# Performance work log

Hardware: AMD Instinct MI355X
Metric: run time of the kernel (lower is better)

Reference implementation:

```python
import jax, jax.numpy as jnp
import numpy as np
from jax.ops import segment_sum, segment_max

D = 64; H = 2; L = 3
N = 50000; G = 128; E = 600000; NE = 300000
EPS_GEN = 1e-7; EPS_LN = 1e-5


def _lin(key, fan_in, shape):
    return jax.random.normal(key, shape, jnp.float32) / np.sqrt(fan_in)


def setup_inputs() -> dict:
    key = jax.random.key(0)
    ks = iter(jax.random.split(key, 40))
    HD = H * D
    inp = {}
    inp['x'] = jax.random.normal(next(ks), (N, D), jnp.float32)
    inp['cond'] = jax.random.normal(next(ks), (G, D), jnp.float32)
    inp['edge_attr'] = jax.random.normal(next(ks), (E, D), jnp.float32)
    inp['edge_index'] = jax.random.randint(next(ks), (2, E), 0, N)
    inp['non_edge_index'] = jax.random.randint(next(ks), (2, NE), 0, N)
    inp['batch'] = jnp.sort(jax.random.randint(next(ks), (N,), 0, G))
    # per-layer stacked params (L leading dim)
    inp['gen_w'] = _lin(next(ks), D, (L, D, D)); inp['gen_b'] = 0.01 * jax.random.normal(next(ks), (L, D), jnp.float32)
    inp['q_w'] = _lin(next(ks), 2 * D, (L, 2 * D, HD)); inp['q_b'] = 0.01 * jax.random.normal(next(ks), (L, HD), jnp.float32)
    inp['k_w'] = _lin(next(ks), 2 * D, (L, 2 * D, HD)); inp['k_b'] = 0.01 * jax.random.normal(next(ks), (L, HD), jnp.float32)
    inp['v_w'] = _lin(next(ks), 2 * D, (L, 2 * D, HD)); inp['v_b'] = 0.01 * jax.random.normal(next(ks), (L, HD), jnp.float32)
    inp['e_w'] = _lin(next(ks), D, (L, D, HD))  # lin_edge has no bias in TransformerConv
    inp['skip_w'] = _lin(next(ks), 2 * D, (L, 2 * D, HD)); inp['skip_b'] = 0.01 * jax.random.normal(next(ks), (L, HD), jnp.float32)
    inp['lin_w'] = _lin(next(ks), HD, (L, HD, D)); inp['lin_b'] = 0.01 * jax.random.normal(next(ks), (L, D), jnp.float32)
    inp['ff_w1'] = _lin(next(ks), D, (L, D, 4 * D)); inp['ff_b1'] = 0.01 * jax.random.normal(next(ks), (L, 4 * D), jnp.float32)
    inp['ff_w2'] = _lin(next(ks), 4 * D, (L, 4 * D, D)); inp['ff_b2'] = 0.01 * jax.random.normal(next(ks), (L, D), jnp.float32)
    return inp


def graph_layernorm(x, batch, num_graphs):
    # PyG LayerNorm(mode='graph', affine=False): mean/var over all nodes AND features of each graph
    cnt = segment_sum(jnp.ones((x.shape[0],), x.dtype), batch, num_segments=num_graphs)
    norm = jnp.maximum(cnt, 1.0) * x.shape[-1]  # [G]
    mean = segment_sum(x, batch, num_segments=num_graphs).sum(-1) / norm
    xc = x - mean[batch][:, None]
    var = segment_sum(xc * xc, batch, num_segments=num_graphs).sum(-1) / norm
    return xc / jnp.sqrt(var + EPS_LN)[batch][:, None]


def gen_conv(x, src, dst, e, w, b, n):
    # GENConv(d,d,num_layers=1,aggr='add',norm=None): mlp(sum_j relu(x_j + e_ij) + eps  +  x_i)
    msg = jax.nn.relu(x[src] + e) + EPS_GEN
    agg = segment_sum(msg, dst, num_segments=n)
    return (agg + x) @ w + b


def trans_conv(x, src, dst, e, qw, qb, kw, kb, vw, vb, ew, sw, sb, n):
    # TransformerConv(2d, d, heads=H, edge_dim=d, concat=True, root_weight=True)
    q = (x @ qw + qb).reshape(n, H, D)
    k = (x @ kw + kb).reshape(n, H, D)
    v = (x @ vw + vb).reshape(n, H, D)
    ee = (e @ ew).reshape(-1, H, D)
    kj = k[src] + ee
    alpha = jnp.einsum('ehd,ehd->eh', q[dst], kj) / np.sqrt(D)  # [E,H]
    m = segment_max(alpha, dst, num_segments=n)
    a = jnp.exp(alpha - m[dst])
    s = segment_sum(a, dst, num_segments=n)
    a = a / (s[dst] + 1e-16)
    msg = (v[src] + ee) * a[..., None]
    out = segment_sum(msg.reshape(-1, H * D), dst, num_segments=n)
    return out + x @ sw + sb


def _forward(x, cond, edge_attr, gen_w, gen_b, q_w, q_b, k_w, k_b, v_w, v_b, e_w,
             skip_w, skip_b, lin_w, lin_b, ff_w1, ff_b1, ff_w2, ff_b2,
             edge_index, non_edge_index, batch):
    n, d = x.shape
    g = cond.shape[0]
    n_aug = n + g
    x_aug = jnp.concatenate([x, cond], 0)
    u = jnp.arange(n)
    v = batch + n
    src0 = jnp.concatenate([edge_index[0], u, v])
    dst0 = jnp.concatenate([edge_index[1], v, u])
    e_p = jnp.zeros((2 * n, d), x.dtype).at[:, 0].set(1.0)
    e_base = jnp.concatenate([edge_attr, e_p], 0)
    # add_self_loops with fill_value='mean': mean of incoming edge attrs per node
    cnt = segment_sum(jnp.ones((src0.shape[0],), x.dtype), dst0, num_segments=n_aug)
    loop_attr = segment_sum(e_base, dst0, num_segments=n_aug) / jnp.maximum(cnt, 1.0)[:, None]
    loops = jnp.arange(n_aug)
    src = jnp.concatenate([src0, loops])
    dst = jnp.concatenate([dst0, loops])
    e_aug = jnp.concatenate([e_base, loop_attr], 0)
    aug_batch = jnp.concatenate([batch, jnp.arange(g)])

    h = x_aug
    for i in range(L):
        hn = graph_layernorm(h, aug_batch, g)
        agg = gen_conv(hn, src, dst, e_aug, gen_w[i], gen_b[i], n_aug)
        cat = jnp.concatenate([hn, agg], 1)  # [n_aug, 2d]
        t = trans_conv(cat, src, dst, e_aug, q_w[i], q_b[i], k_w[i], k_b[i],
                       v_w[i], v_b[i], e_w[i], skip_w[i], skip_b[i], n_aug)
        lh = t @ lin_w[i] + lin_b[i]
        ln2 = graph_layernorm(lh, aug_batch, g)
        ff = jax.nn.leaky_relu(ln2 @ ff_w1[i] + ff_b1[i], 0.01) @ ff_w2[i] + ff_b2[i]
        h = h + ff

    n_emb = h[:n]
    v_emb = h[n:]
    cnt_n = segment_sum(jnp.ones((n,), x.dtype), batch, num_segments=g)
    glob = segment_sum(n_emb, batch, num_segments=g) / jnp.maximum(cnt_n, 1.0)[:, None] + v_emb
    ne_emb = n_emb[non_edge_index[0]] + n_emb[non_edge_index[1]]
    return n_emb, glob, ne_emb


def reference(x, cond, edge_attr, edge_index, non_edge_index, batch, gen_w, gen_b,
              q_w, q_b, k_w, k_b, v_w, v_b, e_w, skip_w, skip_b, lin_w, lin_b,
              ff_w1, ff_b1, ff_w2, ff_b2):
    return _forward(x, cond, edge_attr, gen_w, gen_b, q_w, q_b, k_w, k_b, v_w, v_b,
                    e_w, skip_w, skip_b, lin_w, lin_b, ff_w1, ff_b1, ff_w2, ff_b2,
                    edge_index, non_edge_index, batch)
```

## Files before the change

kernel.cpp:

```cpp
#include <hip/hip_runtime.h>
#include <cstdint>

#define DD 64
#define HH 2
#define LAY 3
#define NN 50000
#define GG 128
#define EE 600000
#define NEE 300000
#define NAUG (NN + GG)
#define E2 (EE + 2 * NN)
#define ESZ (E2 + NAUG)
#define EPS_GEN_F 1e-7f
#define EPS_LN_F 1e-5f
#define SCAN_B 1024
#define NBLK ((NAUG + SCAN_B - 1) / SCAN_B)


__device__ __forceinline__ float2 ld2(const float* p) {
  return *reinterpret_cast<const float2*>(p);
}
__device__ __forceinline__ void st2(float* p, float x, float y) {
  *reinterpret_cast<float2*>(p) = make_float2(x, y);
}

__device__ __forceinline__ float half_sum(float v) {
#pragma unroll
  for (int off = 16; off; off >>= 1) v += __shfl_xor(v, off);
  return v;
}

__device__ __forceinline__ float2 ea2_val(int e, int hl, const float* __restrict__ ea,
                                          const float* __restrict__ la) {
  if (e < EE) return ld2(ea + (size_t)e * DD + 2 * hl);
  if (e < E2) return make_float2((hl == 0) ? 1.0f : 0.0f, 0.0f);
  return ld2(la + (size_t)(e - E2) * DD + 2 * hl);
}

__device__ __forceinline__ int dst_of(int e, const int* __restrict__ ei1,
                                      const int* __restrict__ batch) {
  if (e < EE) return ei1[e];
  if (e < EE + NN) return batch[e - EE] + NN;
  if (e < E2) return e - (EE + NN);
  return e - E2;
}
__device__ __forceinline__ int src_of(int e, const int* __restrict__ ei0,
                                      const int* __restrict__ batch) {
  if (e < EE) return ei0[e];
  if (e < EE + NN) return e - EE;
  if (e < E2) return batch[e - (EE + NN)] + NN;
  return e - E2;
}


__global__ void hist_k(const int* __restrict__ ei1, const int* __restrict__ batch,
                       int* __restrict__ deg) {
  for (int e = blockIdx.x * blockDim.x + threadIdx.x; e < ESZ; e += gridDim.x * blockDim.x)
    atomicAdd(&deg[dst_of(e, ei1, batch)], 1);
}

__global__ __launch_bounds__(SCAN_B) void scan1_k(const int* __restrict__ deg,
                                                  int* __restrict__ rowst,
                                                  int* __restrict__ bsum) {
  __shared__ int buf[SCAN_B];
  int i = blockIdx.x * SCAN_B + threadIdx.x;
  int v = (i < NAUG) ? deg[i] : 0;
  buf[threadIdx.x] = v;
  __syncthreads();
  int acc = v;
#pragma unroll
  for (int off = 1; off < SCAN_B; off <<= 1) {
    int t = (threadIdx.x >= off) ? buf[threadIdx.x - off] : 0;
    __syncthreads();
    buf[threadIdx.x] = acc = acc + t;
    __syncthreads();
  }
  if (i < NAUG) rowst[i] = acc - v;
  if (threadIdx.x == SCAN_B - 1) bsum[blockIdx.x] = acc;
}

__global__ void scan2_k(const int* __restrict__ bsum, int* __restrict__ bpre,
                        int* __restrict__ rowst) {
  if (threadIdx.x == 0) {
    int run = 0;
    for (int b = 0; b < NBLK; b++) {
      bpre[b] = run;
      run += bsum[b];
    }
    rowst[NAUG] = run;
  }
}

__global__ void scan3_k(int* __restrict__ rowst, const int* __restrict__ bpre) {
  int i = blockIdx.x * blockDim.x + threadIdx.x;
  if (i < NAUG) rowst[i] += bpre[i / SCAN_B];
}

__global__ void scatter_k(const int* __restrict__ ei0, const int* __restrict__ ei1,
                          const int* __restrict__ batch, const int* __restrict__ rowst,
                          int* __restrict__ fill, int* __restrict__ ceid,
                          int* __restrict__ csrc) {
  for (int e = blockIdx.x * blockDim.x + threadIdx.x; e < ESZ; e += gridDim.x * blockDim.x) {
    int dn = dst_of(e, ei1, batch);
    int pos = rowst[dn] + atomicAdd(&fill[dn], 1);
    ceid[pos] = e;
    csrc[pos] = src_of(e, ei0, batch);
  }
}

__global__ void gs_k(const int* __restrict__ batch, int* __restrict__ gs) {
  int i = blockIdx.x * blockDim.x + threadIdx.x;
  if (i >= NN) return;
  int b = batch[i];
  int prev = (i > 0) ? batch[i - 1] : -1;
  for (int g = prev + 1; g <= b; ++g) gs[g] = i;
  if (i == NN - 1)
    for (int g = b + 1; g <= GG; ++g) gs[g] = NN;
}

__global__ void hinit_k(const float4* __restrict__ x, const float4* __restrict__ cond,
                        float4* __restrict__ h) {
  for (int idx = blockIdx.x * blockDim.x + threadIdx.x; idx < NAUG * 16;
       idx += gridDim.x * blockDim.x)
    h[idx] = (idx < NN * 16) ? x[idx] : cond[idx - NN * 16];
}

__global__ __launch_bounds__(256) void loopattr_k(const float* __restrict__ eattr,
                                                  const int* __restrict__ rowst,
                                                  const int* __restrict__ ceid,
                                                  float* __restrict__ la) {
  const int lane = threadIdx.x & 63;
  const int half = lane >> 5, hl = lane & 31;
  const int wv = threadIdx.x >> 6;
  for (int i = blockIdx.x * 4 + wv; i < NAUG; i += gridDim.x * 4) {
    int rs = rowst[i], re = rowst[i + 1];
    float ax = 0.f, ay = 0.f;
    int cnt = 0;
    for (int p = rs + half; p < re; p += 2) {
      int e = ceid[p];
      if (e >= E2) continue;
      cnt++;
      float2 ea = (e < EE) ? ld2(eattr + (size_t)e * DD + 2 * hl)
                           : make_float2((hl == 0) ? 1.0f : 0.0f, 0.0f);
      ax += ea.x;
      ay += ea.y;
    }
    ax += __shfl_xor(ax, 32);
    ay += __shfl_xor(ay, 32);
    cnt += __shfl_xor(cnt, 32);
    if (half == 0) {
      float inv = 1.0f / fmaxf((float)cnt, 1.0f);
      st2(la + (size_t)i * DD + 2 * hl, ax * inv, ay * inv);
    }
  }
}


__global__ __launch_bounds__(256) void ln_stats_k(const float* __restrict__ xin,
                                                  const int* __restrict__ gs,
                                                  float* __restrict__ mean,
                                                  float* __restrict__ rstd) {
  __shared__ float red[256];
  __shared__ float mu_s;
  int g = blockIdx.x;
  int s = gs[g], e = gs[g + 1];
  int cnt = e - s + 1;
  int nel = cnt * DD;
  float norm = (float)nel;
  float acc = 0.f;
  for (int idx = threadIdx.x; idx < nel; idx += 256) {
    int loc = idx >> 6;
    int node = (loc < cnt - 1) ? (s + loc) : (NN + g);
    acc += xin[(size_t)node * DD + (idx & 63)];
  }
  red[threadIdx.x] = acc;
  __syncthreads();
  for (int o = 128; o; o >>= 1) {
    if (threadIdx.x < o) red[threadIdx.x] += red[threadIdx.x + o];
    __syncthreads();
  }
  if (threadIdx.x == 0) mu_s = red[0] / norm;
  __syncthreads();
  float mu = mu_s;
  acc = 0.f;
  for (int idx = threadIdx.x; idx < nel; idx += 256) {
    int loc = idx >> 6;
    int node = (loc < cnt - 1) ? (s + loc) : (NN + g);
    float d = xin[(size_t)node * DD + (idx & 63)] - mu;
    acc += d * d;
  }
  __syncthreads();
  red[threadIdx.x] = acc;
  __syncthreads();
  for (int o = 128; o; o >>= 1) {
    if (threadIdx.x < o) red[threadIdx.x] += red[threadIdx.x + o];
    __syncthreads();
  }
  if (threadIdx.x == 0) {
    mean[g] = mu;
    rstd[g] = rsqrtf(red[0] / norm + EPS_LN_F);
  }
}

__global__ void ln_apply_k(const float* __restrict__ xin, const int* __restrict__ batch,
                           const float* __restrict__ mean, const float* __restrict__ rstd,
                           float* __restrict__ o1, float* __restrict__ o2) {
  for (int idx = blockIdx.x * blockDim.x + threadIdx.x; idx < NAUG * 32;
       idx += gridDim.x * blockDim.x) {
    int i = idx >> 5, d2 = idx & 31;
    int g = (i < NN) ? batch[i] : (i - NN);
    float mu = mean[g], rs = rstd[g];
    float2 v = ld2(xin + (size_t)i * DD + 2 * d2);
    float vx = (v.x - mu) * rs, vy = (v.y - mu) * rs;
    st2(o1 + (size_t)i * DD + 2 * d2, vx, vy);
    if (o2) st2(o2 + (size_t)i * 128 + 2 * d2, vx, vy);
  }
}

__global__ __launch_bounds__(256) void gen_node_k(const float* __restrict__ hn,
                                                  const int* __restrict__ rowst,
                                                  const int* __restrict__ ceid,
                                                  const int* __restrict__ csrc,
                                                  const float* __restrict__ eattr,
                                                  const float* __restrict__ la,
                                                  float* __restrict__ gin) {
  const int lane = threadIdx.x & 63;
  const int half = lane >> 5, hl = lane & 31;
  const int wv = threadIdx.x >> 6;
  for (int i = blockIdx.x * 4 + wv; i < NAUG; i += gridDim.x * 4) {
    int rs = rowst[i], re = rowst[i + 1];
    float ax = 0.f, ay = 0.f;
    for (int p = rs + half; p < re; p += 2) {
      int j = csrc[p], e = ceid[p];
      float2 ea = ea2_val(e, hl, eattr, la);
      float2 hv = ld2(hn + (size_t)j * DD + 2 * hl);
      ax += fmaxf(hv.x + ea.x, 0.f);
      ay += fmaxf(hv.y + ea.y, 0.f);
    }
    ax += __shfl_xor(ax, 32);
    ay += __shfl_xor(ay, 32);
    if (half == 0) {
      float2 hme = ld2(hn + (size_t)i * DD + 2 * hl);
      float epsterm = (float)(re - rs) * EPS_GEN_F;
      st2(gin + (size_t)i * DD + 2 * hl, ax + epsterm + hme.x, ay + epsterm + hme.y);
    }
  }
}

template <int IN, int OUT, int ACT, bool ACCUM>
__global__ __launch_bounds__(256) void gemm_k(const float* __restrict__ A,
                                              const float* __restrict__ W,
                                              const float* __restrict__ bias,
                                              float* __restrict__ C, int ldc, int coff) {
  __shared__ float sW[IN * OUT];
  for (int idx = threadIdx.x; idx < IN * OUT; idx += 256) sW[idx] = W[idx];
  __syncthreads();
  const int lane = threadIdx.x & 63;
  const int wv = threadIdx.x >> 6;
  constexpr int AR = IN / 64, CR = OUT / 64;
  for (int row = blockIdx.x * 4 + wv; row < NAUG; row += gridDim.x * 4) {
    float a[AR];
#pragma unroll
    for (int r = 0; r < AR; r++) a[r] = A[(size_t)row * IN + r * 64 + lane];
    float acc[CR];
#pragma unroll
    for (int c = 0; c < CR; c++) acc[c] = bias ? bias[c * 64 + lane] : 0.f;
#pragma unroll
    for (int r = 0; r < AR; r++) {
#pragma unroll
      for (int kk = 0; kk < 64; kk++) {
        float av = __shfl(a[r], kk);
#pragma unroll
        for (int c = 0; c < CR; c++) acc[c] += av * sW[(r * 64 + kk) * OUT + c * 64 + lane];
      }
    }
#pragma unroll
    for (int c = 0; c < CR; c++) {
      float o = acc[c];
      if (ACT == 1) o = (o > 0.f) ? o : 0.01f * o;
      float* p = C + (size_t)row * ldc + coff + c * 64 + lane;
      if (ACCUM)
        *p += o;
      else
        *p = o;
    }
  }
}

__global__ __launch_bounds__(256) void qe_k(const float* __restrict__ q,
                                            const float* __restrict__ ew,
                                            float* __restrict__ qe) {
  __shared__ float sT[128 * 64];
  for (int idx = threadIdx.x; idx < 64 * 128; idx += 256) {
    int c = idx >> 7, kk = idx & 127;
    sT[kk * 64 + c] = ew[idx];
  }
  __syncthreads();
  const int lane = threadIdx.x & 63;
  const int wv = threadIdx.x >> 6;
  for (int i = blockIdx.x * 4 + wv; i < NAUG; i += gridDim.x * 4) {
    float a0 = q[(size_t)i * 128 + lane];
    float a1 = q[(size_t)i * 128 + 64 + lane];
    float acc0 = 0.f, acc1 = 0.f;
#pragma unroll
    for (int d = 0; d < 64; d++) {
      float v0 = __shfl(a0, d), v1 = __shfl(a1, d);
      acc0 += v0 * sT[d * 64 + lane];
      acc1 += v1 * sT[(64 + d) * 64 + lane];
    }
    qe[(size_t)i * 128 + lane] = acc0;
    qe[(size_t)i * 128 + 64 + lane] = acc1;
  }
}

__global__ void wbd_k(const float* __restrict__ ew, float* __restrict__ wbd) {
  int idx = blockIdx.x * 256 + threadIdx.x;
  if (idx >= 128 * 128) return;
  int k = idx >> 7, o = idx & 127;
  wbd[idx] = ((k >> 6) == (o >> 6)) ? ew[(k & 63) * 128 + o] : 0.f;
}

__global__ __launch_bounds__(256) void attn_k(
    const float* __restrict__ q, const float* __restrict__ k, const float* __restrict__ v,
    const float* __restrict__ qe, const int* __restrict__ rowst, const int* __restrict__ ceid,
    const int* __restrict__ csrc, const float* __restrict__ eattr, const float* __restrict__ la,
    float* __restrict__ outv, float* __restrict__ z) {
  const int lane = threadIdx.x & 63;
  const int hl = lane & 31;
  const int wv = threadIdx.x >> 6;
  for (int i = blockIdx.x * 4 + wv; i < NAUG; i += gridDim.x * 4) {
    const int rs = rowst[i], re = rowst[i + 1];
    float2 q2 = ld2(q + (size_t)i * 128 + 2 * lane);
    float2 e2 = ld2(qe + (size_t)i * 128 + 2 * lane);
    float m = -1e30f, s = 0.f;
    float avx = 0.f, avy = 0.f, azx = 0.f, azy = 0.f;
    for (int p = rs; p < re; ++p) {
      int j = csrc[p], e = ceid[p];
      float2 ea = ea2_val(e, hl, eattr, la);
      float2 k2 = ld2(k + (size_t)j * 128 + 2 * lane);
      float2 v2 = ld2(v + (size_t)j * 128 + 2 * lane);
      float part = q2.x * k2.x + q2.y * k2.y + e2.x * ea.x + e2.y * ea.y;
      float a = half_sum(part) * 0.125f;
      float nm = fmaxf(m, a);
      float c = __expf(m - nm), w = __expf(a - nm);
      m = nm;
      s = s * c + w;
      avx = avx * c + w * v2.x;
      avy = avy * c + w * v2.y;
      azx = azx * c + w * ea.x;
      azy = azy * c + w * ea.y;
    }
    float inv = 1.0f / (s + 1e-16f);
    st2(outv + (size_t)i * 128 + 2 * lane, avx * inv, avy * inv);
    st2(z + (size_t)i * 128 + 2 * lane, azx * inv, azy * inv);
  }
}


__global__ void nemb_k(const float4* __restrict__ h, float4* __restrict__ out) {
  for (int idx = blockIdx.x * blockDim.x + threadIdx.x; idx < NN * 16;
       idx += gridDim.x * blockDim.x)
    out[idx] = h[idx];
}

__global__ __launch_bounds__(256) void glob_k(const float* __restrict__ h,
                                              const int* __restrict__ gs,
                                              float* __restrict__ out) {
  __shared__ float part[4][64];
  int g = blockIdx.x;
  int d = threadIdx.x & 63, sub = threadIdx.x >> 6;
  int s = gs[g], e = gs[g + 1];
  float acc = 0.f;
  for (int node = s + sub; node < e; node += 4) acc += h[(size_t)node * DD + d];
  part[sub][d] = acc;
  __syncthreads();
  if (sub == 0) {
    float t = part[0][d] + part[1][d] + part[2][d] + part[3][d];
    t /= fmaxf((float)(e - s), 1.0f);
    t += h[(size_t)(NN + g) * DD + d];
    out[(size_t)NN * DD + (size_t)g * DD + d] = t;
  }
}

__global__ void ne_k(const float4* __restrict__ h4, const int* __restrict__ a,
                     const int* __restrict__ b, float4* __restrict__ out4) {
  const size_t base = (size_t)(NN + GG) * 16;
  for (size_t idx = blockIdx.x * blockDim.x + threadIdx.x; idx < (size_t)NEE * 16;
       idx += (size_t)gridDim.x * blockDim.x) {
    int r = (int)(idx >> 4), c = (int)(idx & 15);
    float4 va = h4[(size_t)a[r] * 16 + c];
    float4 vb = h4[(size_t)b[r] * 16 + c];
    out4[base + idx] = make_float4(va.x + vb.x, va.y + vb.y, va.z + vb.z, va.w + vb.w);
  }
}


extern "C" void kernel_launch(void* const* d_in, const int* in_sizes, int n_in, void* d_out,
                              int out_size, void* d_ws, size_t ws_size, hipStream_t stream) {
  const float* x = (const float*)d_in[0];
  const float* cond = (const float*)d_in[1];
  const float* eattr = (const float*)d_in[2];
  const int* eidx = (const int*)d_in[3];
  const int* neidx = (const int*)d_in[4];
  const int* batch = (const int*)d_in[5];
  const float* gen_w = (const float*)d_in[6];
  const float* gen_b = (const float*)d_in[7];
  const float* q_w = (const float*)d_in[8];
  const float* q_b = (const float*)d_in[9];
  const float* k_w = (const float*)d_in[10];
  const float* k_b = (const float*)d_in[11];
  const float* v_w = (const float*)d_in[12];
  const float* v_b = (const float*)d_in[13];
  const float* e_w = (const float*)d_in[14];
  const float* skip_w = (const float*)d_in[15];
  const float* skip_b = (const float*)d_in[16];
  const float* lin_w = (const float*)d_in[17];
  const float* lin_b = (const float*)d_in[18];
  const float* ff_w1 = (const float*)d_in[19];
  const float* ff_b1 = (const float*)d_in[20];
  const float* ff_w2 = (const float*)d_in[21];
  const float* ff_b2 = (const float*)d_in[22];
  float* out = (float*)d_out;

  size_t off = 0;
  auto alloc = [&](size_t bytes) -> void* {
    void* p = (char*)d_ws + off;
    off += (bytes + 255) & ~(size_t)255;
    return p;
  };
  float* h = (float*)alloc((size_t)NAUG * 64 * 4);
  float* la = (float*)alloc((size_t)NAUG * 64 * 4);
  float* hn = (float*)alloc((size_t)NAUG * 64 * 4);
  float* cat = (float*)alloc((size_t)NAUG * 128 * 4);
  float* qb_ = (float*)alloc((size_t)NAUG * 128 * 4);
  float* kb_ = (float*)alloc((size_t)NAUG * 128 * 4);
  float* vb_ = (float*)alloc((size_t)NAUG * 128 * 4);
  float* qeb = (float*)alloc((size_t)NAUG * 128 * 4);
  float* ob = (float*)alloc((size_t)NAUG * 128 * 4);
  float* zb = (float*)alloc((size_t)NAUG * 128 * 4);
  int* deg = (int*)alloc((size_t)NAUG * 4);
  int* fill = (int*)alloc((size_t)NAUG * 4);
  int* rowst = (int*)alloc((size_t)(NAUG + 1) * 4);
  int* ceid = (int*)alloc((size_t)ESZ * 4);
  int* csrc = (int*)alloc((size_t)ESZ * 4);
  int* gs = (int*)alloc((size_t)(GG + 1) * 4);
  int* bsum = (int*)alloc((size_t)NBLK * 4);
  int* bpre = (int*)alloc((size_t)(NBLK + 1) * 4);
  float* mean = (float*)alloc(GG * 4);
  float* rstd = (float*)alloc(GG * 4);
  float* wbd = (float*)alloc(128 * 128 * 4);
  (void)ws_size;

  hipMemsetAsync(deg, 0, (size_t)NAUG * 4, stream);
  hist_k<<<1024, 256, 0, stream>>>(eidx + EE, batch, deg);
  scan1_k<<<NBLK, SCAN_B, 0, stream>>>(deg, rowst, bsum);
  scan2_k<<<1, 64, 0, stream>>>(bsum, bpre, rowst);
  scan3_k<<<(NAUG + 255) / 256, 256, 0, stream>>>(rowst, bpre);
  hipMemsetAsync(fill, 0, (size_t)NAUG * 4, stream);
  scatter_k<<<1024, 256, 0, stream>>>(eidx, eidx + EE, batch, rowst, fill, ceid, csrc);
  gs_k<<<(NN + 255) / 256, 256, 0, stream>>>(batch, gs);
  hinit_k<<<2048, 256, 0, stream>>>((const float4*)x, (const float4*)cond, (float4*)h);
  loopattr_k<<<2048, 256, 0, stream>>>(eattr, rowst, ceid, la);

  for (int l = 0; l < LAY; l++) {
    const float* gw = gen_w + (size_t)l * 64 * 64;
    const float* gb = gen_b + (size_t)l * 64;
    const float* qw = q_w + (size_t)l * 128 * 128;
    const float* qbia = q_b + (size_t)l * 128;
    const float* kw = k_w + (size_t)l * 128 * 128;
    const float* kbia = k_b + (size_t)l * 128;
    const float* vw = v_w + (size_t)l * 128 * 128;
    const float* vbia = v_b + (size_t)l * 128;
    const float* ew = e_w + (size_t)l * 64 * 128;
    const float* sw = skip_w + (size_t)l * 128 * 128;
    const float* sb = skip_b + (size_t)l * 128;
    const float* lw = lin_w + (size_t)l * 128 * 64;
    const float* lb = lin_b + (size_t)l * 64;
    const float* f1w = ff_w1 + (size_t)l * 64 * 256;
    const float* f1b = ff_b1 + (size_t)l * 256;
    const float* f2w = ff_w2 + (size_t)l * 256 * 64;
    const float* f2b = ff_b2 + (size_t)l * 64;

    ln_stats_k<<<GG, 256, 0, stream>>>(h, gs, mean, rstd);
    ln_apply_k<<<2048, 256, 0, stream>>>(h, batch, mean, rstd, hn, cat);
    gen_node_k<<<2048, 256, 0, stream>>>(hn, rowst, ceid, csrc, eattr, la, zb);
    gemm_k<64, 64, 0, false><<<1024, 256, 0, stream>>>(zb, gw, gb, cat, 128, 64);
    gemm_k<128, 128, 0, false><<<1024, 256, 0, stream>>>(cat, qw, qbia, qb_, 128, 0);
    gemm_k<128, 128, 0, false><<<1024, 256, 0, stream>>>(cat, kw, kbia, kb_, 128, 0);
    gemm_k<128, 128, 0, false><<<1024, 256, 0, stream>>>(cat, vw, vbia, vb_, 128, 0);
    qe_k<<<2048, 256, 0, stream>>>(qb_, ew, qeb);
    attn_k<<<2048, 256, 0, stream>>>(qb_, kb_, vb_, qeb, rowst, ceid, csrc, eattr, la, ob, zb);
    wbd_k<<<64, 256, 0, stream>>>(ew, wbd);
    gemm_k<128, 128, 0, true><<<1024, 256, 0, stream>>>(cat, sw, sb, ob, 128, 0);
    gemm_k<128, 128, 0, true><<<1024, 256, 0, stream>>>(zb, wbd, nullptr, ob, 128, 0);
    gemm_k<128, 64, 0, false><<<1024, 256, 0, stream>>>(ob, lw, lb, hn, 64, 0);
    ln_stats_k<<<GG, 256, 0, stream>>>(hn, gs, mean, rstd);
    ln_apply_k<<<2048, 256, 0, stream>>>(hn, batch, mean, rstd, kb_, nullptr);
    gemm_k<64, 256, 1, false><<<1024, 256, 0, stream>>>(kb_, f1w, f1b, vb_, 256, 0);
    gemm_k<256, 64, 0, true><<<1024, 256, 0, stream>>>(vb_, f2w, f2b, h, 64, 0);
  }

  nemb_k<<<2048, 256, 0, stream>>>((const float4*)h, (float4*)out);
  glob_k<<<GG, 256, 0, stream>>>(h, gs, out);
  ne_k<<<8192, 256, 0, stream>>>((const float4*)h, neidx, neidx + NEE, (float4*)out);
}
```

Baseline: 8.694 ms.

## Split virtual-node work into block kernels, interleave K/V, and tile GEMM rows

Virtual nodes (one per graph, with very high in-degree) move from single-wave loops into dedicated 512-thread block kernels for aggregation and attention, with a cross-wave softmax merge, so their long serial loops no longer stall the grid. K and V are written interleaved into one buffer so attention reads both with one float4 load. The GEMM now handles four rows per wave with float2 weight loads and vectorised staging into shared memory, and the q·We projection becomes a GEMM against a block-diagonal weight. Layer-norm stats use a single pass (E[x²]−μ²), which is faster but less numerically stable. The GEMM row tiling assumes NAUG is a multiple of 4 (50128 is), and the virtual-node self-loop attribute is now computed analytically.

```diff
diff --git a/kernel.cpp b/kernel.cpp
--- a/kernel.cpp
+++ b/kernel.cpp
@@ -20,6 +20,9 @@
 __device__ __forceinline__ float2 ld2(const float* p) {
   return *reinterpret_cast<const float2*>(p);
 }
+__device__ __forceinline__ float4 ld4(const float* p) {
+  return *reinterpret_cast<const float4*>(p);
+}
 __device__ __forceinline__ void st2(float* p, float x, float y) {
   *reinterpret_cast<float2*>(p) = make_float2(x, y);
 }
@@ -125,14 +128,14 @@
     h[idx] = (idx < NN * 16) ? x[idx] : cond[idx - NN * 16];
 }
 
-__global__ __launch_bounds__(256) void loopattr_k(const float* __restrict__ eattr,
-                                                  const int* __restrict__ rowst,
-                                                  const int* __restrict__ ceid,
-                                                  float* __restrict__ la) {
+__global__ __launch_bounds__(256) void loopattr_u_k(const float* __restrict__ eattr,
+                                                    const int* __restrict__ rowst,
+                                                    const int* __restrict__ ceid,
+                                                    float* __restrict__ la) {
   const int lane = threadIdx.x & 63;
   const int half = lane >> 5, hl = lane & 31;
   const int wv = threadIdx.x >> 6;
-  for (int i = blockIdx.x * 4 + wv; i < NAUG; i += gridDim.x * 4) {
+  for (int i = blockIdx.x * 4 + wv; i < NN; i += gridDim.x * 4) {
     int rs = rowst[i], re = rowst[i + 1];
     float ax = 0.f, ay = 0.f;
     int cnt = 0;
@@ -155,50 +158,48 @@
   }
 }
 
+__global__ void la_v_k(const int* __restrict__ gs, float* __restrict__ la) {
+  int idx = blockIdx.x * blockDim.x + threadIdx.x;
+  if (idx >= GG * DD) return;
+  int g = idx >> 6, d = idx & 63;
+  float v = (d == 0 && gs[g + 1] > gs[g]) ? 1.0f : 0.0f;
+  la[(size_t)(NN + g) * DD + d] = v;
+}
+
 
 __global__ __launch_bounds__(256) void ln_stats_k(const float* __restrict__ xin,
                                                   const int* __restrict__ gs,
                                                   float* __restrict__ mean,
                                                   float* __restrict__ rstd) {
-  __shared__ float red[256];
-  __shared__ float mu_s;
+  __shared__ float red[256], red2[256];
   int g = blockIdx.x;
   int s = gs[g], e = gs[g + 1];
   int cnt = e - s + 1;
   int nel = cnt * DD;
   float norm = (float)nel;
-  float acc = 0.f;
+  float acc = 0.f, acc2 = 0.f;
   for (int idx = threadIdx.x; idx < nel; idx += 256) {
     int loc = idx >> 6;
     int node = (loc < cnt - 1) ? (s + loc) : (NN + g);
-    acc += xin[(size_t)node * DD + (idx & 63)];
+    float v = xin[(size_t)node * DD + (idx & 63)];
+    acc += v;
+    acc2 += v * v;
   }
   red[threadIdx.x] = acc;
+  red2[threadIdx.x] = acc2;
   __syncthreads();
   for (int o = 128; o; o >>= 1) {
-    if (threadIdx.x < o) red[threadIdx.x] += red[threadIdx.x + o];
+    if (threadIdx.x < o) {
+      red[threadIdx.x] += red[threadIdx.x + o];
+      red2[threadIdx.x] += red2[threadIdx.x + o];
+    }
     __syncthreads();
   }
-  if (threadIdx.x == 0) mu_s = red[0] / norm;
-  __syncthreads();
-  float mu = mu_s;
-  acc = 0.f;
-  for (int idx = threadIdx.x; idx < nel; idx += 256) {
-    int loc = idx >> 6;
-    int node = (loc < cnt - 1) ? (s + loc) : (NN + g);
-    float d = xin[(size_t)node * DD + (idx & 63)] - mu;
-    acc += d * d;
-  }
-  __syncthreads();
-  red[threadIdx.x] = acc;
-  __syncthreads();
-  for (int o = 128; o; o >>= 1) {
-    if (threadIdx.x < o) red[threadIdx.x] += red[threadIdx.x + o];
-    __syncthreads();
-  }
   if (threadIdx.x == 0) {
+    float mu = red[0] / norm;
+    float var = red2[0] / norm - mu * mu;
     mean[g] = mu;
-    rstd[g] = rsqrtf(red[0] / norm + EPS_LN_F);
+    rstd[g] = rsqrtf(fmaxf(var, 0.f) + EPS_LN_F);
   }
 }
 
@@ -217,17 +218,17 @@
   }
 }
 
-__global__ __launch_bounds__(256) void gen_node_k(const float* __restrict__ hn,
-                                                  const int* __restrict__ rowst,
-                                                  const int* __restrict__ ceid,
-                                                  const int* __restrict__ csrc,
-                                                  const float* __restrict__ eattr,
-                                                  const float* __restrict__ la,
-                                                  float* __restrict__ gin) {
+__global__ __launch_bounds__(256) void gen_u_k(const float* __restrict__ hn,
+                                               const int* __restrict__ rowst,
+                                               const int* __restrict__ ceid,
+                                               const int* __restrict__ csrc,
+                                               const float* __restrict__ eattr,
+                                               const float* __restrict__ la,
+                                               float* __restrict__ gin) {
   const int lane = threadIdx.x & 63;
   const int half = lane >> 5, hl = lane & 31;
   const int wv = threadIdx.x >> 6;
-  for (int i = blockIdx.x * 4 + wv; i < NAUG; i += gridDim.x * 4) {
+  for (int i = blockIdx.x * 4 + wv; i < NN; i += gridDim.x * 4) {
     int rs = rowst[i], re = rowst[i + 1];
     float ax = 0.f, ay = 0.f;
     for (int p = rs + half; p < re; p += 2) {
@@ -247,70 +248,140 @@
   }
 }
 
+__global__ __launch_bounds__(512) void gen_v_k(const float* __restrict__ hn,
+                                               const int* __restrict__ rowst,
+                                               const int* __restrict__ ceid,
+                                               const int* __restrict__ csrc,
+                                               const float* __restrict__ eattr,
+                                               const float* __restrict__ la,
+                                               float* __restrict__ gin) {
+  __shared__ float sacc[8][64];
+  const int lane = threadIdx.x & 63;
+  const int half = lane >> 5, hl = lane & 31;
+  const int wv = threadIdx.x >> 6;
+  const int i = NN + blockIdx.x;
+  const int rs = rowst[i], re = rowst[i + 1];
+  float ax = 0.f, ay = 0.f;
+  for (int p = rs + (wv * 2 + half); p < re; p += 16) {
+    int j = csrc[p], e = ceid[p];
+    float2 ea = ea2_val(e, hl, eattr, la);
+    float2 hv = ld2(hn + (size_t)j * DD + 2 * hl);
+    ax += fmaxf(hv.x + ea.x, 0.f);
+    ay += fmaxf(hv.y + ea.y, 0.f);
+  }
+  ax += __shfl_xor(ax, 32);
+  ay += __shfl_xor(ay, 32);
+  if (half == 0) {
+    sacc[wv][2 * hl] = ax;
+    sacc[wv][2 * hl + 1] = ay;
+  }
+  __syncthreads();
+  if (threadIdx.x < 64) {
+    float t = 0.f;
+#pragma unroll
+    for (int w = 0; w < 8; w++) t += sacc[w][threadIdx.x];
+    gin[(size_t)i * DD + threadIdx.x] =
+        t + (float)(re - rs) * EPS_GEN_F + hn[(size_t)i * DD + threadIdx.x];
+  }
+}
+
 template <int IN, int OUT, int ACT, bool ACCUM>
 __global__ __launch_bounds__(256) void gemm_k(const float* __restrict__ A,
                                               const float* __restrict__ W,
                                               const float* __restrict__ bias,
-                                              float* __restrict__ C, int ldc, int coff) {
-  __shared__ float sW[IN * OUT];
-  for (int idx = threadIdx.x; idx < IN * OUT; idx += 256) sW[idx] = W[idx];
+                                              float* __restrict__ C, int ldc, int coff,
+                                              int pstride, int poff) {
+  __shared__ alignas(16) float sW[IN * OUT];
+  for (int idx = threadIdx.x * 4; idx < IN * OUT; idx += 256 * 4)
+    *reinterpret_cast<float4*>(&sW[idx]) = *reinterpret_cast<const float4*>(&W[idx]);
   __syncthreads();
   const int lane = threadIdx.x & 63;
   const int wv = threadIdx.x >> 6;
-  constexpr int AR = IN / 64, CR = OUT / 64;
-  for (int row = blockIdx.x * 4 + wv; row < NAUG; row += gridDim.x * 4) {
-    float a[AR];
-#pragma unroll
-    for (int r = 0; r < AR; r++) a[r] = A[(size_t)row * IN + r * 64 + lane];
-    float acc[CR];
-#pragma unroll
-    for (int c = 0; c < CR; c++) acc[c] = bias ? bias[c * 64 + lane] : 0.f;
-#pragma unroll
-    for (int r = 0; r < AR; r++) {
-#pragma unroll
-      for (int kk = 0; kk < 64; kk++) {
-        float av = __shfl(a[r], kk);
-#pragma unroll
-        for (int c = 0; c < CR; c++) acc[c] += av * sW[(r * 64 + kk) * OUT + c * 64 + lane];
+  constexpr int AR = IN / 64;
+  constexpr int NP = OUT / 128;
+  const int gw = blockIdx.x * 4 + wv;
+  const int nw = gridDim.x * 4;
+  for (int row0 = gw * 4; row0 < NAUG; row0 += nw * 4) {
+    float a[4][AR];
+#pragma unroll
+    for (int rr = 0; rr < 4; rr++)
+#pragma unroll
+      for (int r = 0; r < AR; r++) a[rr][r] = A[(size_t)(row0 + rr) * IN + r * 64 + lane];
+    if constexpr (OUT == 64) {
+      float acc[4];
+#pragma unroll
+      for (int rr = 0; rr < 4; rr++) acc[rr] = bias ? bias[lane] : 0.f;
+#pragma unroll
+      for (int r = 0; r < AR; r++)
+#pragma unroll
+        for (int kk = 0; kk < 64; kk++) {
+          float w = sW[(r * 64 + kk) * OUT + lane];
+#pragma unroll
+          for (int rr = 0; rr < 4; rr++) acc[rr] += __shfl(a[rr][r], kk) * w;
+        }
+#pragma unroll
+      for (int rr = 0; rr < 4; rr++) {
+        float o = acc[rr];
+        if (ACT == 1) o = (o > 0.f) ? o : 0.01f * o;
+        float* p = C + (size_t)(row0 + rr) * ldc + coff + lane;
+        if (ACCUM)
+          *p += o;
+        else
+          *p = o;
       }
-    }
-#pragma unroll
-    for (int c = 0; c < CR; c++) {
-      float o = acc[c];
-      if (ACT == 1) o = (o > 0.f) ? o : 0.01f * o;
-      float* p = C + (size_t)row * ldc + coff + c * 64 + lane;
-      if (ACCUM)
-        *p += o;
-      else
-        *p = o;
-    }
-  }
-}
-
-__global__ __launch_bounds__(256) void qe_k(const float* __restrict__ q,
-                                            const float* __restrict__ ew,
-                                            float* __restrict__ qe) {
-  __shared__ float sT[128 * 64];
-  for (int idx = threadIdx.x; idx < 64 * 128; idx += 256) {
-    int c = idx >> 7, kk = idx & 127;
-    sT[kk * 64 + c] = ew[idx];
-  }
-  __syncthreads();
-  const int lane = threadIdx.x & 63;
-  const int wv = threadIdx.x >> 6;
-  for (int i = blockIdx.x * 4 + wv; i < NAUG; i += gridDim.x * 4) {
-    float a0 = q[(size_t)i * 128 + lane];
-    float a1 = q[(size_t)i * 128 + 64 + lane];
-    float acc0 = 0.f, acc1 = 0.f;
-#pragma unroll
-    for (int d = 0; d < 64; d++) {
-      float v0 = __shfl(a0, d), v1 = __shfl(a1, d);
-      acc0 += v0 * sT[d * 64 + lane];
-      acc1 += v1 * sT[(64 + d) * 64 + lane];
-    }
-    qe[(size_t)i * 128 + lane] = acc0;
-    qe[(size_t)i * 128 + 64 + lane] = acc1;
-  }
+    } else {
+      float2 acc[4][NP];
+#pragma unroll
+      for (int rr = 0; rr < 4; rr++)
+#pragma unroll
+        for (int pp = 0; pp < NP; pp++)
+          acc[rr][pp] = bias ? ld2(bias + 2 * (lane + 64 * pp)) : make_float2(0.f, 0.f);
+#pragma unroll
+      for (int r = 0; r < AR; r++)
+#pragma unroll
+        for (int kk = 0; kk < 64; kk++) {
+          float2 w[NP];
+#pragma unroll
+          for (int pp = 0; pp < NP; pp++)
+            w[pp] = *reinterpret_cast<const float2*>(
+                &sW[(r * 64 + kk) * OUT + 2 * (lane + 64 * pp)]);
+#pragma unroll
+          for (int rr = 0; rr < 4; rr++) {
+            float av = __shfl(a[rr][r], kk);
+#pragma unroll
+            for (int pp = 0; pp < NP; pp++) {
+              acc[rr][pp].x += av * w[pp].x;
+              acc[rr][pp].y += av * w[pp].y;
+            }
+          }
+        }
+#pragma unroll
+      for (int rr = 0; rr < 4; rr++)
+#pragma unroll
+        for (int pp = 0; pp < NP; pp++) {
+          float2 o = acc[rr][pp];
+          if (ACT == 1) {
+            o.x = (o.x > 0.f) ? o.x : 0.01f * o.x;
+            o.y = (o.y > 0.f) ? o.y : 0.01f * o.y;
+          }
+          float* p = C + (size_t)(row0 + rr) * ldc + coff + (lane + 64 * pp) * pstride + poff;
+          if (ACCUM) {
+            float2 old = ld2(p);
+            st2(p, old.x + o.x, old.y + o.y);
+          } else {
+            st2(p, o.x, o.y);
+          }
+        }
+    }
+  }
+}
+
+__global__ void wqe_k(const float* __restrict__ ew, float* __restrict__ wqe) {
+  int idx = blockIdx.x * 256 + threadIdx.x;
+  if (idx >= 128 * 128) return;
+  int kcol = idx >> 7, ocol = idx & 127;
+  int h = kcol >> 6, c = kcol & 63, h2 = ocol >> 6, d = ocol & 63;
+  wqe[idx] = (h == h2) ? ew[d * 128 + 64 * h + c] : 0.f;
 }
 
 __global__ void wbd_k(const float* __restrict__ ew, float* __restrict__ wbd) {
@@ -320,15 +391,15 @@
   wbd[idx] = ((k >> 6) == (o >> 6)) ? ew[(k & 63) * 128 + o] : 0.f;
 }
 
-__global__ __launch_bounds__(256) void attn_k(
-    const float* __restrict__ q, const float* __restrict__ k, const float* __restrict__ v,
-    const float* __restrict__ qe, const int* __restrict__ rowst, const int* __restrict__ ceid,
-    const int* __restrict__ csrc, const float* __restrict__ eattr, const float* __restrict__ la,
-    float* __restrict__ outv, float* __restrict__ z) {
+__global__ __launch_bounds__(256) void attn_u_k(
+    const float* __restrict__ q, const float* __restrict__ kv, const float* __restrict__ qe,
+    const int* __restrict__ rowst, const int* __restrict__ ceid, const int* __restrict__ csrc,
+    const float* __restrict__ eattr, const float* __restrict__ la, float* __restrict__ outv,
+    float* __restrict__ z) {
   const int lane = threadIdx.x & 63;
   const int hl = lane & 31;
   const int wv = threadIdx.x >> 6;
-  for (int i = blockIdx.x * 4 + wv; i < NAUG; i += gridDim.x * 4) {
+  for (int i = blockIdx.x * 4 + wv; i < NN; i += gridDim.x * 4) {
     const int rs = rowst[i], re = rowst[i + 1];
     float2 q2 = ld2(q + (size_t)i * 128 + 2 * lane);
     float2 e2 = ld2(qe + (size_t)i * 128 + 2 * lane);
@@ -337,22 +408,81 @@
     for (int p = rs; p < re; ++p) {
       int j = csrc[p], e = ceid[p];
       float2 ea = ea2_val(e, hl, eattr, la);
-      float2 k2 = ld2(k + (size_t)j * 128 + 2 * lane);
-      float2 v2 = ld2(v + (size_t)j * 128 + 2 * lane);
-      float part = q2.x * k2.x + q2.y * k2.y + e2.x * ea.x + e2.y * ea.y;
+      float4 kv4 = ld4(kv + (size_t)j * 256 + 4 * lane);
+      float part = q2.x * kv4.x + q2.y * kv4.y + e2.x * ea.x + e2.y * ea.y;
       float a = half_sum(part) * 0.125f;
       float nm = fmaxf(m, a);
       float c = __expf(m - nm), w = __expf(a - nm);
       m = nm;
       s = s * c + w;
-      avx = avx * c + w * v2.x;
-      avy = avy * c + w * v2.y;
+      avx = avx * c + w * kv4.z;
+      avy = avy * c + w * kv4.w;
       azx = azx * c + w * ea.x;
       azy = azy * c + w * ea.y;
     }
     float inv = 1.0f / (s + 1e-16f);
     st2(outv + (size_t)i * 128 + 2 * lane, avx * inv, avy * inv);
     st2(z + (size_t)i * 128 + 2 * lane, azx * inv, azy * inv);
+  }
+}
+
+__global__ __launch_bounds__(512) void attn_v_k(
+    const float* __restrict__ q, const float* __restrict__ kv, const float* __restrict__ qe,
+    const int* __restrict__ rowst, const int* __restrict__ ceid, const int* __restrict__ csrc,
+    const float* __restrict__ eattr, const float* __restrict__ la, float* __restrict__ outv,
+    float* __restrict__ z) {
+  __shared__ float sm[8][2], ss[8][2], sav[8][128], saz[8][128];
+  const int lane = threadIdx.x & 63;
+  const int hl = lane & 31;
+  const int wv = threadIdx.x >> 6;
+  const int i = NN + blockIdx.x;
+  const int rs = rowst[i], re = rowst[i + 1];
+  float2 q2 = ld2(q + (size_t)i * 128 + 2 * lane);
+  float2 e2 = ld2(qe + (size_t)i * 128 + 2 * lane);
+  float m = -1e30f, s = 0.f;
+  float avx = 0.f, avy = 0.f, azx = 0.f, azy = 0.f;
+  for (int p = rs + wv; p < re; p += 8) {
+    int j = csrc[p], e = ceid[p];
+    float2 ea = ea2_val(e, hl, eattr, la);
+    float4 kv4 = ld4(kv + (size_t)j * 256 + 4 * lane);
+    float part = q2.x * kv4.x + q2.y * kv4.y + e2.x * ea.x + e2.y * ea.y;
+    float a = half_sum(part) * 0.125f;
+    float nm = fmaxf(m, a);
+    float c = __expf(m - nm), w = __expf(a - nm);
+    m = nm;
+    s = s * c + w;
+    avx = avx * c + w * kv4.z;
+    avy = avy * c + w * kv4.w;
+    azx = azx * c + w * ea.x;
+    azy = azy * c + w * ea.y;
+  }
+  if (hl == 0) {
+    sm[wv][lane >> 5] = m;
+    ss[wv][lane >> 5] = s;
+  }
+  sav[wv][2 * lane] = avx;
+  sav[wv][2 * lane + 1] = avy;
+  saz[wv][2 * lane] = azx;
+  saz[wv][2 * lane + 1] = azy;
+  __syncthreads();
+  if (wv == 0) {
+    int half = lane >> 5;
+    float M = -1e30f;
+#pragma unroll
+    for (int w = 0; w < 8; w++) M = fmaxf(M, sm[w][half]);
+    float stot = 0.f, AVX = 0.f, AVY = 0.f, AZX = 0.f, AZY = 0.f;
+#pragma unroll
+    for (int w = 0; w < 8; w++) {
+      float sc = __expf(sm[w][half] - M);
+      stot += ss[w][half] * sc;
+      AVX += sav[w][2 * lane] * sc;
+      AVY += sav[w][2 * lane + 1] * sc;
+      AZX += saz[w][2 * lane] * sc;
+      AZY += saz[w][2 * lane + 1] * sc;
+    }
+    float inv = 1.0f / (stot + 1e-16f);
+    st2(outv + (size_t)i * 128 + 2 * lane, AVX * inv, AVY * inv);
+    st2(z + (size_t)i * 128 + 2 * lane, AZX * inv, AZY * inv);
   }
 }
 
@@ -433,9 +563,8 @@
   float* hn = (float*)alloc((size_t)NAUG * 64 * 4);
   float* cat = (float*)alloc((size_t)NAUG * 128 * 4);
   float* qb_ = (float*)alloc((size_t)NAUG * 128 * 4);
-  float* kb_ = (float*)alloc((size_t)NAUG * 128 * 4);
-  float* vb_ = (float*)alloc((size_t)NAUG * 128 * 4);
   float* qeb = (float*)alloc((size_t)NAUG * 128 * 4);
+  float* kvb = (float*)alloc((size_t)NAUG * 256 * 4);
   float* ob = (float*)alloc((size_t)NAUG * 128 * 4);
   float* zb = (float*)alloc((size_t)NAUG * 128 * 4);
   int* deg = (int*)alloc((size_t)NAUG * 4);
@@ -449,6 +578,7 @@
   float* mean = (float*)alloc(GG * 4);
   float* rstd = (float*)alloc(GG * 4);
   float* wbd = (float*)alloc(128 * 128 * 4);
+  float* wqe = (float*)alloc(128 * 128 * 4);
   (void)ws_size;
 
   hipMemsetAsync(deg, 0, (size_t)NAUG * 4, stream);
@@ -460,7 +590,8 @@
   scatter_k<<<1024, 256, 0, stream>>>(eidx, eidx + EE, batch, rowst, fill, ceid, csrc);
   gs_k<<<(NN + 255) / 256, 256, 0, stream>>>(batch, gs);
   hinit_k<<<2048, 256, 0, stream>>>((const float4*)x, (const float4*)cond, (float4*)h);
-  loopattr_k<<<2048, 256, 0, stream>>>(eattr, rowst, ceid, la);
+  loopattr_u_k<<<2048, 256, 0, stream>>>(eattr, rowst, ceid, la);
+  la_v_k<<<32, 256, 0, stream>>>(gs, la);
 
   for (int l = 0; l < LAY; l++) {
     const float* gw = gen_w + (size_t)l * 64 * 64;
@@ -483,21 +614,24 @@
 
     ln_stats_k<<<GG, 256, 0, stream>>>(h, gs, mean, rstd);
     ln_apply_k<<<2048, 256, 0, stream>>>(h, batch, mean, rstd, hn, cat);
-    gen_node_k<<<2048, 256, 0, stream>>>(hn, rowst, ceid, csrc, eattr, la, zb);
-    gemm_k<64, 64, 0, false><<<1024, 256, 0, stream>>>(zb, gw, gb, cat, 128, 64);
-    gemm_k<128, 128, 0, false><<<1024, 256, 0, stream>>>(cat, qw, qbia, qb_, 128, 0);
-    gemm_k<128, 128, 0, false><<<1024, 256, 0, stream>>>(cat, kw, kbia, kb_, 128, 0);
-    gemm_k<128, 128, 0, false><<<1024, 256, 0, stream>>>(cat, vw, vbia, vb_, 128, 0);
-    qe_k<<<2048, 256, 0, stream>>>(qb_, ew, qeb);
-    attn_k<<<2048, 256, 0, stream>>>(qb_, kb_, vb_, qeb, rowst, ceid, csrc, eattr, la, ob, zb);
+    gen_u_k<<<2048, 256, 0, stream>>>(hn, rowst, ceid, csrc, eattr, la, zb);
+    gen_v_k<<<GG, 512, 0, stream>>>(hn, rowst, ceid, csrc, eattr, la, zb);
+    gemm_k<64, 64, 0, false><<<1024, 256, 0, stream>>>(zb, gw, gb, cat, 128, 64, 2, 0);
+    gemm_k<128, 128, 0, false><<<1024, 256, 0, stream>>>(cat, qw, qbia, qb_, 128, 0, 2, 0);
+    wqe_k<<<64, 256, 0, stream>>>(ew, wqe);
+    gemm_k<128, 128, 0, false><<<1024, 256, 0, stream>>>(qb_, wqe, nullptr, qeb, 128, 0, 2, 0);
+    gemm_k<128, 128, 0, false><<<1024, 256, 0, stream>>>(cat, kw, kbia, kvb, 256, 0, 4, 0);
+    gemm_k<128, 128, 0, false><<<1024, 256, 0, stream>>>(cat, vw, vbia, kvb, 256, 0, 4, 2);
+    attn_u_k<<<2048, 256, 0, stream>>>(qb_, kvb, qeb, rowst, ceid, csrc, eattr, la, ob, zb);
+    attn_v_k<<<GG, 512, 0, stream>>>(qb_, kvb, qeb, rowst, ceid, csrc, eattr, la, ob, zb);
     wbd_k<<<64, 256, 0, stream>>>(ew, wbd);
-    gemm_k<128, 128, 0, true><<<1024, 256, 0, stream>>>(cat, sw, sb, ob, 128, 0);
-    gemm_k<128, 128, 0, true><<<1024, 256, 0, stream>>>(zb, wbd, nullptr, ob, 128, 0);
-    gemm_k<128, 64, 0, false><<<1024, 256, 0, stream>>>(ob, lw, lb, hn, 64, 0);
+    gemm_k<128, 128, 0, true><<<1024, 256, 0, stream>>>(cat, sw, sb, ob, 128, 0, 2, 0);
+    gemm_k<128, 128, 0, true><<<1024, 256, 0, stream>>>(zb, wbd, nullptr, ob, 128, 0, 2, 0);
+    gemm_k<128, 64, 0, false><<<1024, 256, 0, stream>>>(ob, lw, lb, hn, 64, 0, 2, 0);
     ln_stats_k<<<GG, 256, 0, stream>>>(hn, gs, mean, rstd);
-    ln_apply_k<<<2048, 256, 0, stream>>>(hn, batch, mean, rstd, kb_, nullptr);
-    gemm_k<64, 256, 1, false><<<1024, 256, 0, stream>>>(kb_, f1w, f1b, vb_, 256, 0);
-    gemm_k<256, 64, 0, true><<<1024, 256, 0, stream>>>(vb_, f2w, f2b, h, 64, 0);
+    ln_apply_k<<<2048, 256, 0, stream>>>(hn, batch, mean, rstd, qb_, nullptr);
+    gemm_k<64, 256, 1, false><<<1024, 256, 0, stream>>>(qb_, f1w, f1b, kvb, 256, 0, 2, 0);
+    gemm_k<256, 64, 0, true><<<1024, 256, 0, stream>>>(kvb, f2w, f2b, h, 64, 0, 2, 0);
   }
 
   nemb_k<<<2048, 256, 0, stream>>>((const float4*)h, (float4*)out);
```

New measurement: 12.80 ms. 1.47x slower.
